# Optimization experiments

Measured on AMD Instinct MI355X. Metric: run time of the kernel, lower is better.

## Reference

```python
import jax, jax.numpy as jnp
import numpy as np

B, N, D_IN, H, L, HEADS = 8, 1024, 64, 128, 2, 4
HEAD_DIM = H // HEADS
EPS = 1e-5


def setup_inputs() -> dict:
    key = jax.random.key(0)
    ks = jax.random.split(key, 20)
    x = jax.random.normal(ks[0], (B, N, D_IN), dtype=jnp.float32)
    adj = jax.random.randint(ks[1], (B, N, N), 0, 2).astype(jnp.float32)
    s = lambda fan_in: 1.0 / np.sqrt(fan_in)
    enc_w = jax.random.uniform(ks[2], (H, D_IN), minval=-s(D_IN), maxval=s(D_IN))
    enc_b = jax.random.uniform(ks[3], (H,), minval=-s(D_IN), maxval=s(D_IN))
    # per-layer stacked projection weights, torch Linear layout [out,in]
    def mk(k, shape):
        return jax.random.uniform(k, shape, minval=-s(H), maxval=s(H))
    q_w = mk(ks[4], (L, H, H)); q_b = mk(ks[5], (L, H))
    k_w = mk(ks[6], (L, H, H)); k_b = mk(ks[7], (L, H))
    v_w = mk(ks[8], (L, H, H)); v_b = mk(ks[9], (L, H))
    o_w = mk(ks[10], (L, H, H)); o_b = mk(ks[11], (L, H))
    ln_g = jnp.ones((L, H), jnp.float32)
    ln_b = jnp.zeros((L, H), jnp.float32)
    out_w = mk(ks[12], (H, H)); out_b = mk(ks[13], (H,))
    return {"x": x, "adj": adj, "enc_w": enc_w, "enc_b": enc_b,
            "q_w": q_w, "q_b": q_b, "k_w": k_w, "k_b": k_b,
            "v_w": v_w, "v_b": v_b, "o_w": o_w, "o_b": o_b,
            "ln_g": ln_g, "ln_b": ln_b, "out_w": out_w, "out_b": out_b}


def _layernorm(x, g, b):
    mu = jnp.mean(x, axis=-1, keepdims=True)
    var = jnp.var(x, axis=-1, keepdims=True)
    return (x - mu) * jax.lax.rsqrt(var + EPS) * g + b


def _gat_layer(h, adj, qw, qb, kw, kb, vw, vb, ow, ob):
    b, n, _ = h.shape
    q = (h @ qw.T + qb).reshape(b, n, HEADS, HEAD_DIM)
    k = (h @ kw.T + kb).reshape(b, n, HEADS, HEAD_DIM)
    v = (h @ vw.T + vb).reshape(b, n, HEADS, HEAD_DIM)
    scale = HEAD_DIM ** -0.5
    attn = jnp.einsum('bihd,bjhd->bhij', q, k) * scale
    mask = adj[:, None, :, :]  # (b,1,n,n)
    attn = jnp.where(mask == 0, -jnp.inf, attn)
    a = jax.nn.softmax(attn, axis=-1)
    a = jnp.nan_to_num(a, nan=0.0)  # rows with no neighbours -> 0
    out = jnp.einsum('bhij,bjhd->bihd', a, v).reshape(b, n, H)
    return out @ ow.T + ob


def reference(x, adj, enc_w, enc_b, q_w, q_b, k_w, k_b, v_w, v_b,
              o_w, o_b, ln_g, ln_b, out_w, out_b):
    h = jax.nn.relu(x @ enc_w.T + enc_b)
    for i in range(L):
        h_new = _gat_layer(h, adj, q_w[i], q_b[i], k_w[i], k_b[i],
                           v_w[i], v_b[i], o_w[i], o_b[i])
        h = jax.nn.relu(_layernorm(h_new, ln_g[i], ln_b[i])) + h
    return h @ out_w.T + out_b
```

## Files before the change

### kernel.cpp

```cpp
#include <hip/hip_runtime.h>

#define B 8
#define N 1024
#define D_IN 64
#define H 128
#define HEADS 4
#define HD 32
#define L 2
#define EPS 1e-5f
#define NEG_BIG -1e30f
#define QSCALE (0.17677669529663687f * 1.4426950408889634f)

typedef __attribute__((ext_vector_type(8))) short bf16x8;
typedef __attribute__((ext_vector_type(4))) float f32x4;

__device__ __forceinline__ unsigned short f2bf(float f) {
    unsigned u = __float_as_uint(f);
    u = u + 0x7fffu + ((u >> 16) & 1u);
    return (unsigned short)(u >> 16);
}
__device__ __forceinline__ float bf2f(unsigned short s) {
    return __uint_as_float(((unsigned)s) << 16);
}
__device__ __forceinline__ void gload_lds16(const void* g, void* l) {
    __builtin_amdgcn_global_load_lds(
        (const __attribute__((address_space(1))) unsigned int*)g,
        (__attribute__((address_space(3))) unsigned int*)l,
        16, 0, 0);
}

#define NPACK 1024
#define NPREP 579
#define NENC  256

__global__ __launch_bounds__(256) void front_kernel(
    const float* __restrict__ adj, const float* __restrict__ x,
    const float* __restrict__ enc_w, const float* __restrict__ eb,
    const float* __restrict__ q_w, const float* __restrict__ k_w,
    const float* __restrict__ v_w, const float* __restrict__ q_b,
    const float* __restrict__ k_b, const float* __restrict__ v_b,
    const float* __restrict__ o_w, const float* __restrict__ out_w,
    unsigned* __restrict__ mb, unsigned short* __restrict__ wqkv,
    float* __restrict__ bqkv, unsigned short* __restrict__ woh,
    unsigned short* __restrict__ wol, unsigned short* __restrict__ wfh,
    unsigned short* __restrict__ wfl, float* __restrict__ h,
    unsigned short* __restrict__ h_bf) {
    __shared__ unsigned short wt[H * D_IN];
    __shared__ unsigned short at[32 * D_IN];
    const int blk = blockIdx.x;
    const int t = threadIdx.x;

    if (blk < NPACK) {
        int wd = blk * 256 + t;
        const float4* src = (const float4*)(adj + (size_t)wd * 32);
        unsigned m = 0;
        #pragma unroll
        for (int c = 0; c < 8; ++c) {
            float4 f = src[c];
            if (f.x != 0.0f) m |= 1u << (c * 4 + 0);
            if (f.y != 0.0f) m |= 1u << (c * 4 + 1);
            if (f.z != 0.0f) m |= 1u << (c * 4 + 2);
            if (f.w != 0.0f) m |= 1u << (c * 4 + 3);
        }
        mb[wd] = m;
        return;
    }
    if (blk < NPACK + NPREP) {
        int id = (blk - NPACK) * 256 + t;
        const int WQ = L * 3 * H * H;
        const int BQ = L * 3 * H;
        const int WO = L * H * H;
        if (id < WQ) {
            int layer = id / (3 * H * H);
            int r = id % (3 * H * H);
            int mat = r / (H * H);
            int e = r % (H * H);
            const float* src = mat == 0 ? q_w : (mat == 1 ? k_w : v_w);
            float f = src[layer * H * H + e];
            if (mat == 0) f *= QSCALE;
            wqkv[id] = f2bf(f);
            return;
        }
        id -= WQ;
        if (id < BQ) {
            int layer = id / (3 * H);
            int r = id % (3 * H);
            int mat = r / H;
            int e = r % H;
            const float* src = mat == 0 ? q_b : (mat == 1 ? k_b : v_b);
            float f = src[layer * H + e];
            if (mat == 0) f *= QSCALE;
            bqkv[id] = f;
            return;
        }
        id -= BQ;
        if (id < WO) {
            float f = o_w[id];
            unsigned short hi = f2bf(f);
            woh[id] = hi;
            wol[id] = f2bf(f - bf2f(hi));
            return;
        }
        id -= WO;
        {
            float f = out_w[id];
            unsigned short hi = f2bf(f);
            wfh[id] = hi;
            wfl[id] = f2bf(f - bf2f(hi));
        }
        return;
    }
    const int r0 = (blk - NPACK - NPREP) * 32;
    const int w = t >> 6, lane = t & 63, g = lane >> 4, c16 = lane & 15;
    const int rw = w & 1, chw = w >> 1;

    #pragma unroll
    for (int i = 0; i < 8; ++i) {
        int idx4 = i * 256 + t;
        int row = idx4 >> 4, c4 = (idx4 & 15) * 4;
        float4 f = ((const float4*)enc_w)[idx4];
        int off = row * 64 + (((c4 >> 3) ^ (row & 7)) * 8) + (c4 & 7);
        wt[off] = f2bf(f.x); wt[off + 1] = f2bf(f.y);
        wt[off + 2] = f2bf(f.z); wt[off + 3] = f2bf(f.w);
    }
    #pragma unroll
    for (int i = 0; i < 2; ++i) {
        int idx4 = i * 256 + t;
        int row = idx4 >> 4, c4 = (idx4 & 15) * 4;
        float4 f = ((const float4*)(x + (size_t)r0 * D_IN))[idx4];
        int off = row * 64 + (((c4 >> 3) ^ (row & 7)) * 8) + (c4 & 7);
        at[off] = f2bf(f.x); at[off + 1] = f2bf(f.y);
        at[off + 2] = f2bf(f.z); at[off + 3] = f2bf(f.w);
    }
    __syncthreads();

    const int arow = rw * 16 + c16;
    bf16x8 a0 = *(const bf16x8*)(at + arow * 64 + ((g ^ (arow & 7)) * 8));
    bf16x8 a1 = *(const bf16x8*)(at + arow * 64 + (((4 + g) ^ (arow & 7)) * 8));
    f32x4 acc[4];
    #pragma unroll
    for (int sub = 0; sub < 4; ++sub) {
        int bcol = chw * 64 + sub * 16 + c16;
        bf16x8 b0 = *(const bf16x8*)(wt + bcol * 64 + ((g ^ (bcol & 7)) * 8));
        bf16x8 b1 = *(const bf16x8*)(wt + bcol * 64 + (((4 + g) ^ (bcol & 7)) * 8));
        f32x4 z = {0.f, 0.f, 0.f, 0.f};
        z = __builtin_amdgcn_mfma_f32_16x16x32_bf16(a0, b0, z, 0, 0, 0);
        acc[sub] = __builtin_amdgcn_mfma_f32_16x16x32_bf16(a1, b1, z, 0, 0, 0);
    }
    #pragma unroll
    for (int sub = 0; sub < 4; ++sub) {
        int col = chw * 64 + sub * 16 + c16;
        float bias = eb[col];
        #pragma unroll
        for (int rr = 0; rr < 4; ++rr) {
            int row = r0 + rw * 16 + g * 4 + rr;
            float v = fmaxf(acc[sub][rr] + bias, 0.0f);
            h[(size_t)row * H + col] = v;
            h_bf[(size_t)row * H + col] = f2bf(v);
        }
    }
}

__global__ __launch_bounds__(256) void qkv_kernel(
    const unsigned short* __restrict__ h_bf, const unsigned short* __restrict__ wqkv_l,
    const float* __restrict__ bqkv_l,
    unsigned short* __restrict__ q, unsigned short* __restrict__ k,
    unsigned short* __restrict__ vT) {
    __shared__ unsigned short wt[192 * 128];
    __shared__ unsigned short at[64 * 128];
    const int t = threadIdx.x;
    const int r0 = (blockIdx.x >> 1) * 64;
    const int ch = blockIdx.x & 1;
    const int w = t >> 6, lane = t & 63, g = lane >> 4, c16 = lane & 15;
    const unsigned short* wsrc = wqkv_l + (size_t)ch * 192 * 128;

    #pragma unroll
    for (int i = 0; i < 12; ++i) {
        int ci = i * 256 + t, row = ci >> 4, cr = ci & 15;
        gload_lds16(wsrc + (size_t)row * 128 + (cr ^ (row & 7)) * 8,
                    (char*)wt + (i * 4 + w) * 1024);
    }
    #pragma unroll
    for (int i = 0; i < 4; ++i) {
        int ci = i * 256 + t, row = ci >> 4, cr = ci & 15;
        gload_lds16(h_bf + (size_t)(r0 + row) * 128 + (cr ^ (row & 7)) * 8,
                    (char*)at + (i * 4 + w) * 1024);
    }
    __syncthreads();

    const int arow = w * 16 + c16;
    bf16x8 a[4];
    #pragma unroll
    for (int ks = 0; ks < 4; ++ks)
        a[ks] = *(const bf16x8*)(at + arow * 128 + (((ks * 4 + g) ^ (arow & 7)) * 8));

    f32x4 acc[12];
    #pragma unroll
    for (int sub = 0; sub < 12; ++sub) {
        int bcol = sub * 16 + c16;
        f32x4 z = {0.f, 0.f, 0.f, 0.f};
        #pragma unroll
        for (int ks = 0; ks < 4; ++ks) {
            bf16x8 bb = *(const bf16x8*)(wt + (size_t)bcol * 128 + (((ks * 4 + g) ^ (bcol & 7)) * 8));
            z = __builtin_amdgcn_mfma_f32_16x16x32_bf16(a[ks], bb, z, 0, 0, 0);
        }
        acc[sub] = z;
    }
    #pragma unroll
    for (int sub = 0; sub < 12; ++sub) {
        int gcol = ch * 192 + sub * 16 + c16;
        int mat = gcol >> 7;
        int colin = gcol & 127;
        float bias = bqkv_l[mat * H + colin];
        if (mat < 2) {
            unsigned short* dst = mat == 0 ? q : k;
            #pragma unroll
            for (int rr = 0; rr < 4; ++rr) {
                int row = r0 + w * 16 + g * 4 + rr;
                dst[(size_t)row * H + colin] = f2bf(acc[sub][rr] + bias);
            }
        } else {
            int hd = colin >> 5, d = colin & 31;
            int bb = r0 >> 10;
            int jbase = (r0 & (N - 1)) + w * 16 + g * 4;
            int pos = (jbase & ~63) + ((((jbase >> 3) & 7) ^ (d & 7)) << 3) + (jbase & 7);
            float v0 = acc[sub][0] + bias, v1 = acc[sub][1] + bias;
            float v2 = acc[sub][2] + bias, v3 = acc[sub][3] + bias;
            unsigned lo, hi;
            asm("v_cvt_pk_bf16_f32 %0, %1, %2" : "=v"(lo) : "v"(v0), "v"(v1));
            asm("v_cvt_pk_bf16_f32 %0, %1, %2" : "=v"(hi) : "v"(v2), "v"(v3));
            uint2 pk2; pk2.x = lo; pk2.y = hi;
            *(uint2*)(vT + ((size_t)(bb * HEADS + hd) * HD + d) * N + pos) = pk2;
        }
    }
}

__global__ __launch_bounds__(256) void attn_kernel(
    const unsigned short* __restrict__ qg, const unsigned short* __restrict__ kg,
    const unsigned short* __restrict__ vTg, const unsigned* __restrict__ mb,
    float* __restrict__ ao) {
    __shared__ unsigned short qt[64 * 32];
    __shared__ unsigned short kt[2][128 * 32];
    __shared__ unsigned short vt[2][32 * 128];
    __shared__ unsigned short pl[4][16 * 136];

    const int bid = blockIdx.x;
    const int xcd = bid & 7;
    const int rem = bid >> 3;
    const int itile = rem & 15;
    const int grp = (rem >> 4) * 8 + xcd;
    const int head = grp & 3;
    const int b = grp >> 2;
    const int i0 = itile * 64;
    const int bh = b * HEADS + head;

    const int t = threadIdx.x;
    const int w = t >> 6;
    const int lane = t & 63;
    const int g = lane >> 4;
    const int c16 = lane & 15;

    const int srow = t >> 2;
    const int sch = (t & 3) ^ ((t >> 2) & 3);

    gload_lds16(qg + ((size_t)(b * N + i0 + srow)) * H + head * HD + sch * 8,
                (char*)qt + w * 1024);
    #pragma unroll
    for (int i = 0; i < 2; ++i)
        gload_lds16(kg + ((size_t)(b * N + i * 64 + srow)) * H + head * HD + sch * 8,
                    (char*)kt[0] + i * 4096 + w * 1024);
    #pragma unroll
    for (int i = 0; i < 2; ++i) {
        int d = i * 16 + (t >> 4), c = t & 15;
        gload_lds16(vTg + ((size_t)bh * HD + d) * N + c * 8,
                    (char*)vt[0] + i * 4096 + w * 1024);
    }
    const unsigned* mrow = mb + (size_t)(b * N + i0 + w * 16 + c16) * (N / 32);
    uint4 am = *(const uint4*)mrow;

    __syncthreads();

    const int swq = c16 & 3;
    const bf16x8 qfrag = *(const bf16x8*)(qt + (w * 16 + c16) * 32 + ((g ^ swq) * 8));

    f32x4 oacc[2];
    oacc[0] = (f32x4){0.f, 0.f, 0.f, 0.f};
    oacc[1] = (f32x4){0.f, 0.f, 0.f, 0.f};
    float mrun = NEG_BIG, lrun = 0.0f;

    for (int jt = 0; jt < 8; ++jt) {
        const int cur = jt & 1;
        uint4 amn;
        if (jt < 7) {
            const int j0n = (jt + 1) * 128;
            #pragma unroll
            for (int i = 0; i < 2; ++i)
                gload_lds16(kg + ((size_t)(b * N + j0n + i * 64 + srow)) * H + head * HD + sch * 8,
                            (char*)kt[cur ^ 1] + i * 4096 + w * 1024);
            #pragma unroll
            for (int i = 0; i < 2; ++i) {
                int d = i * 16 + (t >> 4), c = t & 15;
                gload_lds16(vTg + ((size_t)bh * HD + d) * N + j0n + c * 8,
                            (char*)vt[cur ^ 1] + i * 4096 + w * 1024);
            }
            amn = *(const uint4*)(mrow + (jt + 1) * 4);
        }
        f32x4 sacc[8];
        __builtin_amdgcn_s_setprio(1);
        #pragma unroll
        for (int jsub = 0; jsub < 8; ++jsub) {
            bf16x8 kfrag = *(const bf16x8*)(kt[cur] + (jsub * 16 + c16) * 32 + ((g ^ swq) * 8));
            f32x4 z = {0.f, 0.f, 0.f, 0.f};
            sacc[jsub] = __builtin_amdgcn_mfma_f32_16x16x32_bf16(kfrag, qfrag, z, 0, 0, 0);
        }
        __builtin_amdgcn_s_setprio(0);
        float mx = NEG_BIG;
        #pragma unroll
        for (int jsub = 0; jsub < 8; ++jsub) {
            int wsel = jsub >> 1;
            unsigned mw = wsel == 0 ? am.x : wsel == 1 ? am.y : wsel == 2 ? am.z : am.w;
            #pragma unroll
            for (int r = 0; r < 4; ++r) {
                bool alive = (mw >> ((jsub & 1) * 16 + g * 4 + r)) & 1u;
                float s = alive ? sacc[jsub][r] : NEG_BIG;
                sacc[jsub][r] = s;
                mx = fmaxf(mx, s);
            }
        }
        mx = fmaxf(mx, __shfl_xor(mx, 16));
        mx = fmaxf(mx, __shfl_xor(mx, 32));
        float mnew = fmaxf(mrun, mx);
        float sf = exp2f(mrun - mnew);
        mrun = mnew;
        float rs = 0.0f;
        #pragma unroll
        for (int jsub = 0; jsub < 8; ++jsub)
            #pragma unroll
            for (int r = 0; r < 4; ++r) {
                float pv = exp2f(sacc[jsub][r] - mnew);
                sacc[jsub][r] = pv;
                rs += pv;
            }
        rs += __shfl_xor(rs, 16);
        rs += __shfl_xor(rs, 32);
        lrun = lrun * sf + rs;
        #pragma unroll
        for (int jsub = 0; jsub < 8; ++jsub) {
            unsigned lo, hi;
            asm("v_cvt_pk_bf16_f32 %0, %1, %2" : "=v"(lo) : "v"(sacc[jsub][0]), "v"(sacc[jsub][1]));
            asm("v_cvt_pk_bf16_f32 %0, %1, %2" : "=v"(hi) : "v"(sacc[jsub][2]), "v"(sacc[jsub][3]));
            uint2 pk2; pk2.x = lo; pk2.y = hi;
            *(uint2*)(&pl[w][c16 * 136 + jsub * 16 + g * 4]) = pk2;
        }
        #pragma unroll
        for (int dsub = 0; dsub < 2; ++dsub)
            #pragma unroll
            for (int r = 0; r < 4; ++r)
                oacc[dsub][r] *= sf;
        asm volatile("s_waitcnt lgkmcnt(0)" ::: "memory");
        __builtin_amdgcn_s_setprio(1);
        #pragma unroll
        for (int ks = 0; ks < 4; ++ks) {
            bf16x8 pa = *(const bf16x8*)(&pl[w][c16 * 136 + ks * 32 + g * 8]);
            #pragma unroll
            for (int dsub = 0; dsub < 2; ++dsub) {
                int cj = ks * 4 + g;
                bf16x8 va = *(const bf16x8*)(vt[cur] + (dsub * 16 + c16) * 128 +
                                             (cj >> 3) * 64 + (((cj & 7) ^ (c16 & 7)) * 8));
                oacc[dsub] = __builtin_amdgcn_mfma_f32_16x16x32_bf16(va, pa, oacc[dsub], 0, 0, 0);
            }
        }
        __builtin_amdgcn_s_setprio(0);
        if (jt < 7) {
            am = amn;
            __syncthreads();
        }
    }
    float inv = (lrun > 0.0f) ? (1.0f / lrun) : 0.0f;
    #pragma unroll
    for (int dsub = 0; dsub < 2; ++dsub) {
        float4 o;
        o.x = oacc[dsub][0] * inv; o.y = oacc[dsub][1] * inv;
        o.z = oacc[dsub][2] * inv; o.w = oacc[dsub][3] * inv;
        *(float4*)(ao + ((size_t)(b * N + i0 + w * 16 + c16)) * H +
                   head * HD + dsub * 16 + g * 4) = o;
    }
}

__device__ __forceinline__ void stage_split32(
    const float* __restrict__ src, unsigned short* hi, unsigned short* lo, int t) {
    #pragma unroll
    for (int it = 0; it < 4; ++it) {
        int idx4 = it * 256 + t;
        int row = idx4 >> 5, c4 = (idx4 & 31) * 4;
        float4 f = ((const float4*)src)[idx4];
        unsigned short h0 = f2bf(f.x), h1 = f2bf(f.y), h2 = f2bf(f.z), h3 = f2bf(f.w);
        unsigned short l0 = f2bf(f.x - bf2f(h0)), l1 = f2bf(f.y - bf2f(h1));
        unsigned short l2 = f2bf(f.z - bf2f(h2)), l3 = f2bf(f.w - bf2f(h3));
        *(unsigned*)(hi + row * 130 + c4)     = (unsigned)h0 | ((unsigned)h1 << 16);
        *(unsigned*)(hi + row * 130 + c4 + 2) = (unsigned)h2 | ((unsigned)h3 << 16);
        *(unsigned*)(lo + row * 130 + c4)     = (unsigned)l0 | ((unsigned)l1 << 16);
        *(unsigned*)(lo + row * 130 + c4 + 2) = (unsigned)l2 | ((unsigned)l3 << 16);
    }
}

__device__ __forceinline__ void split_gemm4(
    const unsigned short* ah, const unsigned short* al,
    const unsigned short* wh, const unsigned short* wl,
    int arow, int g, int c16, int bcol0, f32x4* acc) {
    bf16x8 ahf[4], alf[4];
    #pragma unroll
    for (int ks = 0; ks < 4; ++ks) {
        ahf[ks] = *(const bf16x8*)(ah + arow * 130 + ks * 32 + g * 8);
        alf[ks] = *(const bf16x8*)(al + arow * 130 + ks * 32 + g * 8);
    }
    #pragma unroll
    for (int sub = 0; sub < 4; ++sub) {
        int bcol = bcol0 + sub * 16 + c16;
        f32x4 z = {0.f, 0.f, 0.f, 0.f};
        #pragma unroll
        for (int ks = 0; ks < 4; ++ks) {
            bf16x8 bh = *(const bf16x8*)(wh + bcol * 128 + (((ks * 4 + g) ^ (bcol & 7)) * 8));
            bf16x8 bl = *(const bf16x8*)(wl + bcol * 128 + (((ks * 4 + g) ^ (bcol & 7)) * 8));
            z = __builtin_amdgcn_mfma_f32_16x16x32_bf16(ahf[ks], bh, z, 0, 0, 0);
            z = __builtin_amdgcn_mfma_f32_16x16x32_bf16(alf[ks], bh, z, 0, 0, 0);
            z = __builtin_amdgcn_mfma_f32_16x16x32_bf16(ahf[ks], bl, z, 0, 0, 0);
        }
        acc[sub] = z;
    }
}

__device__ __forceinline__ void stage_w(const unsigned short* __restrict__ src,
                                        unsigned short* dst, int t, int w) {
    #pragma unroll
    for (int i = 0; i < 8; ++i) {
        int ci = i * 256 + t, row = ci >> 4, cr = ci & 15;
        gload_lds16(src + (size_t)row * 128 + (cr ^ (row & 7)) * 8,
                    (char*)dst + (i * 4 + w) * 1024);
    }
}

__global__ __launch_bounds__(256) void oln_kernel(
    const float* __restrict__ ao, const unsigned short* __restrict__ woh_l,
    const unsigned short* __restrict__ wol_l, const float* __restrict__ ob,
    const float* __restrict__ lng, const float* __restrict__ lnb,
    float* __restrict__ h, unsigned short* __restrict__ h_bf) {
    __shared__ unsigned short ah[32 * 130], al[32 * 130];
    __shared__ unsigned short wh[128 * 128], wl[128 * 128];
    __shared__ float red1[2][32], red2[2][32];
    const int t = threadIdx.x;
    const int r0 = blockIdx.x * 32;
    const int w = t >> 6, lane = t & 63, g = lane >> 4, c16 = lane & 15;
    const int rw = w & 1, chw = w >> 1;

    stage_w(woh_l, wh, t, w);
    stage_w(wol_l, wl, t, w);
    stage_split32(ao + (size_t)r0 * H, ah, al, t);
    __syncthreads();

    const int arow = rw * 16 + c16;
    f32x4 acc[4];
    split_gemm4(ah, al, wh, wl, arow, g, c16, chw * 64, acc);

    float val[4][4], s1[4] = {0, 0, 0, 0}, s2[4] = {0, 0, 0, 0};
    #pragma unroll
    for (int sub = 0; sub < 4; ++sub) {
        int col = chw * 64 + sub * 16 + c16;
        float bias = ob[col];
        #pragma unroll
        for (int rr = 0; rr < 4; ++rr) {
            float vv = acc[sub][rr] + bias;
            val[sub][rr] = vv;
            s1[rr] += vv;
            s2[rr] += vv * vv;
        }
    }
    #pragma unroll
    for (int rr = 0; rr < 4; ++rr) {
        #pragma unroll
        for (int off = 1; off < 16; off <<= 1) {
            s1[rr] += __shfl_xor(s1[rr], off);
            s2[rr] += __shfl_xor(s2[rr], off);
        }
    }
    if (c16 == 0) {
        #pragma unroll
        for (int rr = 0; rr < 4; ++rr) {
            red1[chw][rw * 16 + g * 4 + rr] = s1[rr];
            red2[chw][rw * 16 + g * 4 + rr] = s2[rr];
        }
    }
    __syncthreads();
    #pragma unroll
    for (int rr = 0; rr < 4; ++rr) {
        int rl = rw * 16 + g * 4 + rr;
        float t1 = red1[0][rl] + red1[1][rl];
        float t2 = red2[0][rl] + red2[1][rl];
        float mu = t1 * (1.0f / H);
        float var = t2 * (1.0f / H) - mu * mu;
        float rsn = rsqrtf(var + EPS);
        int row = r0 + rl;
        #pragma unroll
        for (int sub = 0; sub < 4; ++sub) {
            int col = chw * 64 + sub * 16 + c16;
            float y = (val[sub][rr] - mu) * rsn * lng[col] + lnb[col];
            float hn = fmaxf(y, 0.0f) + h[(size_t)row * H + col];
            h[(size_t)row * H + col] = hn;
            h_bf[(size_t)row * H + col] = f2bf(hn);
        }
    }
}

__global__ __launch_bounds__(256) void olnfinal_kernel(
    const float* __restrict__ ao, const unsigned short* __restrict__ woh_l,
    const unsigned short* __restrict__ wol_l, const float* __restrict__ ob,
    const float* __restrict__ lng, const float* __restrict__ lnb,
    const float* __restrict__ h, const unsigned short* __restrict__ wfh,
    const unsigned short* __restrict__ wfl, const float* __restrict__ fb,
    float* __restrict__ out) {
    __shared__ unsigned short ah[32 * 130], al[32 * 130];
    __shared__ unsigned short wh[128 * 128], wl[128 * 128];
    __shared__ float red1[2][32], red2[2][32];
    const int t = threadIdx.x;
    const int r0 = blockIdx.x * 32;
    const int w = t >> 6, lane = t & 63, g = lane >> 4, c16 = lane & 15;
    const int rw = w & 1, chw = w >> 1;

    stage_w(woh_l, wh, t, w);
    stage_w(wol_l, wl, t, w);
    stage_split32(ao + (size_t)r0 * H, ah, al, t);
    __syncthreads();

    const int arow = rw * 16 + c16;
    f32x4 acc[4];
    split_gemm4(ah, al, wh, wl, arow, g, c16, chw * 64, acc);

    float val[4][4], s1[4] = {0, 0, 0, 0}, s2[4] = {0, 0, 0, 0};
    #pragma unroll
    for (int sub = 0; sub < 4; ++sub) {
        int col = chw * 64 + sub * 16 + c16;
        float bias = ob[col];
        #pragma unroll
        for (int rr = 0; rr < 4; ++rr) {
            float vv = acc[sub][rr] + bias;
            val[sub][rr] = vv;
            s1[rr] += vv;
            s2[rr] += vv * vv;
        }
    }
    #pragma unroll
    for (int rr = 0; rr < 4; ++rr) {
        #pragma unroll
        for (int off = 1; off < 16; off <<= 1) {
            s1[rr] += __shfl_xor(s1[rr], off);
            s2[rr] += __shfl_xor(s2[rr], off);
        }
    }
    if (c16 == 0) {
        #pragma unroll
        for (int rr = 0; rr < 4; ++rr) {
            red1[chw][rw * 16 + g * 4 + rr] = s1[rr];
            red2[chw][rw * 16 + g * 4 + rr] = s2[rr];
        }
    }
    __syncthreads();
    #pragma unroll
    for (int rr = 0; rr < 4; ++rr) {
        int rl = rw * 16 + g * 4 + rr;
        float t1 = red1[0][rl] + red1[1][rl];
        float t2 = red2[0][rl] + red2[1][rl];
        float mu = t1 * (1.0f / H);
        float var = t2 * (1.0f / H) - mu * mu;
        float rsn = rsqrtf(var + EPS);
        #pragma unroll
        for (int sub = 0; sub < 4; ++sub) {
            int col = chw * 64 + sub * 16 + c16;
            float y = (val[sub][rr] - mu) * rsn * lng[col] + lnb[col];
            float hn = fmaxf(y, 0.0f) + h[(size_t)(r0 + rl) * H + col];
            unsigned short hi = f2bf(hn);
            ah[rl * 130 + col] = hi;
            al[rl * 130 + col] = f2bf(hn - bf2f(hi));
        }
    }
    stage_w(wfh, wh, t, w);
    stage_w(wfl, wl, t, w);
    __syncthreads();

    f32x4 fac[4];
    split_gemm4(ah, al, wh, wl, arow, g, c16, chw * 64, fac);
    #pragma unroll
    for (int sub = 0; sub < 4; ++sub) {
        int col = chw * 64 + sub * 16 + c16;
        float bias = fb[col];
        #pragma unroll
        for (int rr = 0; rr < 4; ++rr) {
            int row = r0 + rw * 16 + g * 4 + rr;
            out[(size_t)row * H + col] = fac[sub][rr] + bias;
        }
    }
}

extern "C" void kernel_launch(void* const* d_in, const int* in_sizes, int n_in,
                              void* d_out, int out_size, void* d_ws, size_t ws_size,
                              hipStream_t stream) {
    const float* x     = (const float*)d_in[0];
    const float* adj   = (const float*)d_in[1];
    const float* enc_w = (const float*)d_in[2];
    const float* enc_b = (const float*)d_in[3];
    const float* q_w   = (const float*)d_in[4];
    const float* q_b   = (const float*)d_in[5];
    const float* k_w   = (const float*)d_in[6];
    const float* k_b   = (const float*)d_in[7];
    const float* v_w   = (const float*)d_in[8];
    const float* v_b   = (const float*)d_in[9];
    const float* o_w   = (const float*)d_in[10];
    const float* o_b   = (const float*)d_in[11];
    const float* ln_g  = (const float*)d_in[12];
    const float* ln_b  = (const float*)d_in[13];
    const float* out_w = (const float*)d_in[14];
    const float* out_b = (const float*)d_in[15];

    const size_t BNH = (size_t)B * N * H;
    float* h  = (float*)d_ws;
    float* ao = h + BNH;
    unsigned short* h_bf = (unsigned short*)(ao + BNH);
    unsigned short* qb = h_bf + BNH;
    unsigned short* kb = qb + BNH;
    unsigned short* vT = kb + BNH;
    unsigned* mbits = (unsigned*)(vT + BNH);
    unsigned short* wqkv = (unsigned short*)(mbits + (size_t)B * N * N / 32);
    float* bqkv = (float*)(wqkv + (size_t)L * 3 * H * H);
    unsigned short* woh = (unsigned short*)(bqkv + L * 3 * H);
    unsigned short* wol = woh + (size_t)L * H * H;
    unsigned short* wfh = wol + (size_t)L * H * H;
    unsigned short* wfl = wfh + (size_t)H * H;

    front_kernel<<<NPACK + NPREP + NENC, 256, 0, stream>>>(
        adj, x, enc_w, enc_b, q_w, k_w, v_w, q_b, k_b, v_b, o_w, out_w,
        mbits, wqkv, bqkv, woh, wol, wfh, wfl, h, h_bf);

    qkv_kernel<<<B * N / 32, 256, 0, stream>>>(h_bf, wqkv, bqkv, qb, kb, vT);
    attn_kernel<<<B * HEADS * (N / 64), 256, 0, stream>>>(qb, kb, vT, mbits, ao);
    oln_kernel<<<B * N / 32, 256, 0, stream>>>(
        ao, woh, wol, o_b, ln_g, ln_b, h, h_bf);
    qkv_kernel<<<B * N / 32, 256, 0, stream>>>(
        h_bf, wqkv + (size_t)3 * H * H, bqkv + 3 * H, qb, kb, vT);
    attn_kernel<<<B * HEADS * (N / 64), 256, 0, stream>>>(qb, kb, vT, mbits, ao);
    olnfinal_kernel<<<B * N / 32, 256, 0, stream>>>(
        ao, woh + (size_t)H * H, wol + (size_t)H * H, o_b + H,
        ln_g + H, ln_b + H, h, wfh, wfl, out_b, (float*)d_out);
}
```

Measured before the change: 90.66 us.

## Triple-buffer K/V tiles in attention and preload all mask words upfront

The attention kernel moves from double to triple buffering of K and V tiles in LDS, prefetching two tiles ahead. The full barrier is replaced by partial vmcnt waits plus s_barrier, so one tile's loads can stay in flight across iterations. All eight mask uint4 words per row are loaded into registers at the start and the loop is fully unrolled. In exchange the kernel uses more LDS and registers, which may lower occupancy, and correctness depends on the hand-counted vmcnt values.

After: 89.07 us. Within noise of the previous version (-1.8%).

```diff
diff --git a/kernel.cpp b/kernel.cpp
--- a/kernel.cpp
+++ b/kernel.cpp
@@ -240,8 +240,8 @@
     const unsigned short* __restrict__ vTg, const unsigned* __restrict__ mb,
     float* __restrict__ ao) {
     __shared__ unsigned short qt[64 * 32];
-    __shared__ unsigned short kt[2][128 * 32];
-    __shared__ unsigned short vt[2][32 * 128];
+    __shared__ unsigned short kt[3][128 * 32];
+    __shared__ unsigned short vt[3][32 * 128];
     __shared__ unsigned short pl[4][16 * 136];
 
     const int bid = blockIdx.x;
@@ -263,22 +263,29 @@
     const int srow = t >> 2;
     const int sch = (t & 3) ^ ((t >> 2) & 3);
 
+    const unsigned* mrow = mb + (size_t)(b * N + i0 + w * 16 + c16) * (N / 32);
+    uint4 am[8];
+    #pragma unroll
+    for (int jt = 0; jt < 8; ++jt) am[jt] = *(const uint4*)(mrow + jt * 4);
+
     gload_lds16(qg + ((size_t)(b * N + i0 + srow)) * H + head * HD + sch * 8,
                 (char*)qt + w * 1024);
     #pragma unroll
-    for (int i = 0; i < 2; ++i)
-        gload_lds16(kg + ((size_t)(b * N + i * 64 + srow)) * H + head * HD + sch * 8,
-                    (char*)kt[0] + i * 4096 + w * 1024);
-    #pragma unroll
-    for (int i = 0; i < 2; ++i) {
-        int d = i * 16 + (t >> 4), c = t & 15;
-        gload_lds16(vTg + ((size_t)bh * HD + d) * N + c * 8,
-                    (char*)vt[0] + i * 4096 + w * 1024);
-    }
-    const unsigned* mrow = mb + (size_t)(b * N + i0 + w * 16 + c16) * (N / 32);
-    uint4 am = *(const uint4*)mrow;
-
-    __syncthreads();
+    for (int tt = 0; tt < 2; ++tt) {
+        const int j0 = tt * 128;
+        #pragma unroll
+        for (int i = 0; i < 2; ++i)
+            gload_lds16(kg + ((size_t)(b * N + j0 + i * 64 + srow)) * H + head * HD + sch * 8,
+                        (char*)kt[tt] + i * 4096 + w * 1024);
+        #pragma unroll
+        for (int i = 0; i < 2; ++i) {
+            int d = i * 16 + (t >> 4), c = t & 15;
+            gload_lds16(vTg + ((size_t)bh * HD + d) * N + j0 + c * 8,
+                        (char*)vt[tt] + i * 4096 + w * 1024);
+        }
+    }
+    asm volatile("s_waitcnt vmcnt(4)" ::: "memory");
+    __builtin_amdgcn_s_barrier();
 
     const int swq = c16 & 3;
     const bf16x8 qfrag = *(const bf16x8*)(qt + (w * 16 + c16) * 32 + ((g ^ swq) * 8));
@@ -288,22 +295,22 @@
     oacc[1] = (f32x4){0.f, 0.f, 0.f, 0.f};
     float mrun = NEG_BIG, lrun = 0.0f;
 
+    #pragma unroll
     for (int jt = 0; jt < 8; ++jt) {
-        const int cur = jt & 1;
-        uint4 amn;
-        if (jt < 7) {
-            const int j0n = (jt + 1) * 128;
+        const int cur = jt % 3;
+        if (jt < 6) {
+            const int nb = (jt + 2) % 3;
+            const int j0n = (jt + 2) * 128;
             #pragma unroll
             for (int i = 0; i < 2; ++i)
                 gload_lds16(kg + ((size_t)(b * N + j0n + i * 64 + srow)) * H + head * HD + sch * 8,
-                            (char*)kt[cur ^ 1] + i * 4096 + w * 1024);
+                            (char*)kt[nb] + i * 4096 + w * 1024);
             #pragma unroll
             for (int i = 0; i < 2; ++i) {
                 int d = i * 16 + (t >> 4), c = t & 15;
                 gload_lds16(vTg + ((size_t)bh * HD + d) * N + j0n + c * 8,
-                            (char*)vt[cur ^ 1] + i * 4096 + w * 1024);
+                            (char*)vt[nb] + i * 4096 + w * 1024);
             }
-            amn = *(const uint4*)(mrow + (jt + 1) * 4);
         }
         f32x4 sacc[8];
         __builtin_amdgcn_s_setprio(1);
@@ -318,7 +325,8 @@
         #pragma unroll
         for (int jsub = 0; jsub < 8; ++jsub) {
             int wsel = jsub >> 1;
-            unsigned mw = wsel == 0 ? am.x : wsel == 1 ? am.y : wsel == 2 ? am.z : am.w;
+            unsigned mw = wsel == 0 ? am[jt].x : wsel == 1 ? am[jt].y
+                        : wsel == 2 ? am[jt].z : am[jt].w;
             #pragma unroll
             for (int r = 0; r < 4; ++r) {
                 bool alive = (mw >> ((jsub & 1) * 16 + g * 4 + r)) & 1u;
@@ -372,8 +380,9 @@
         }
         __builtin_amdgcn_s_setprio(0);
         if (jt < 7) {
-            am = amn;
-            __syncthreads();
+            if (jt < 6) asm volatile("s_waitcnt vmcnt(4)" ::: "memory");
+            else        asm volatile("s_waitcnt vmcnt(0)" ::: "memory");
+            __builtin_amdgcn_s_barrier();
         }
     }
     float inv = (lrun > 0.0f) ? (1.0f / lrun) : 0.0f;
```
